# Kernel optimization log

Hardware: AMD Instinct MI355X
Metric: run time of the kernel (lower is better)

Reference implementation:

```python
import jax, jax.numpy as jnp
import numpy as np
from jax import lax

B, L, H, K = 64, 1024, 768, 4
C1, C2 = 0.1, 0.1


def crf_marginals(feats, maskf, T):
    """Batched linear-chain CRF forward-backward.
    feats: [B,L,K] emission scores, maskf: [B,L] float (1=valid), T: [K,K] transitions.
    Returns marginals [B,L,K] (zeroed at padded positions)."""
    a0 = feats[:, 0]  # [B,K]

    def fwd_step(a, xs):
        f_t, m_t = xs  # [B,K], [B]
        new = f_t + jax.nn.logsumexp(a[:, :, None] + T[None], axis=1)
        a = jnp.where(m_t[:, None] > 0, new, a)  # freeze alpha past last valid token
        return a, a

    _, alphas_rest = lax.scan(fwd_step, a0,
                              (jnp.swapaxes(feats[:, 1:], 0, 1), maskf[:, 1:].T))
    alphas = jnp.concatenate([a0[None], alphas_rest], axis=0)  # [L,B,K]
    logZ = jax.nn.logsumexp(alphas[-1], axis=-1)  # [B] (alpha frozen at last valid t)

    bL = jnp.zeros_like(a0)

    def bwd_step(b, xs):
        f_n, m_n = xs  # emission/mask at t+1
        new = jax.nn.logsumexp(T[None] + (f_n + b)[:, None, :], axis=2)
        b = jnp.where(m_n[:, None] > 0, new, b)  # beta stays 0 until last valid token
        return b, b

    xs = (jnp.swapaxes(feats[:, 1:][:, ::-1], 0, 1), maskf[:, 1:][:, ::-1].T)
    _, betas_rev = lax.scan(bwd_step, bL, xs)
    betas = jnp.concatenate([bL[None], betas_rev], axis=0)[::-1]  # [L,B,K]

    marg = jnp.exp(alphas + betas - logZ[None, :, None]) * maskf.T[:, :, None]
    return jnp.swapaxes(marg, 0, 1)  # [B,L,K]


def _forward(hidden, maskf, w, b, T):
    feats = hidden @ w.T + b                      # [B,L,K] feat2tri
    marg = crf_marginals(feats, maskf, T)
    sp = marg[:, :, 1]                            # select_polarities, masked [B,L]
    gamma = sp.sum(axis=1) / 2.0                  # [B]
    sent_vs = jnp.einsum('bl,blh->bh', sp, hidden) / gamma[:, None]
    s_prob = sp / gamma[:, None]                  # padded-ragged per-token probs
    s_prob_norm = jnp.abs(s_prob).sum(axis=1).mean()
    pena = jax.nn.relu(T[1, 0] - T[0, 0]) + jax.nn.relu(T[0, 1] - T[1, 1])
    norm_pen = C1 * pena + C2 * s_prob_norm
    return sent_vs, norm_pen, s_prob


def setup_inputs():
    key = jax.random.key(0)
    ks = jax.random.split(key, 8)
    hidden = jax.random.normal(ks[0], (B, L, H), dtype=jnp.float32)
    seq_lens = jax.random.randint(ks[1], (B,), L // 4, L + 1)
    # hidden_mask: 0 for valid tokens, nonzero for padding (forward uses mask = hidden_mask==0)
    hidden_mask = (jnp.arange(L)[None, :] >= seq_lens[:, None]).astype(jnp.int32)
    subj_position = jax.random.randint(ks[2], (B, L), -20, 21)
    obj_position = jax.random.randint(ks[3], (B, L), -20, 21)
    pe_inputs = jax.random.randint(ks[4], (B, L), 0, 2 * L)
    pe_binary = jax.random.randint(ks[5], (B, L), 0, 2)
    w_feat2tri = jax.random.normal(ks[6], (K, H), dtype=jnp.float32) * (1.0 / np.sqrt(H)).astype(np.float32)
    b_feat2tri = jnp.zeros((K,), dtype=jnp.float32)
    transitions = jax.random.normal(ks[7], (K, K), dtype=jnp.float32) * 0.1
    return dict(hidden=hidden, hidden_mask=hidden_mask, subj_position=subj_position,
                obj_position=obj_position, seq_lens=seq_lens, pe_inputs=pe_inputs,
                pe_binary=pe_binary, w_feat2tri=w_feat2tri, b_feat2tri=b_feat2tri,
                transitions=transitions)


def reference(hidden, hidden_mask, subj_position, obj_position, seq_lens, pe_inputs,
              pe_binary, w_feat2tri, b_feat2tri, transitions):
    maskf = (hidden_mask == 0).astype(hidden.dtype)
    # relevance is computed in the original forward but never consumed downstream,
    # so it has no effect on outputs; omitted here.
    return _forward(hidden, maskf, w_feat2tri, b_feat2tri, transitions)
```

## Files before the change

kernel.cpp:

```cpp
#include <hip/hip_runtime.h>

#define B 64
#define L 1024
#define H 768
#define NROWS (B * L)
#define LOG2E 1.4426950408889634f
#define CS 16
#define NCH 64
#define NG 16

#define EXP2(x) __builtin_amdgcn_exp2f(x)
#define LOG2(x) __builtin_amdgcn_logf(x)

__device__ __forceinline__ void renorm4(float& x0, float& x1, float& x2, float& x3, float& lc) {
    const float g = fmaxf(fmaxf(x0, x1), fmaxf(x2, x3));
    const int e = (__float_as_int(g) >> 23) & 255;
    const float s = __int_as_float((254 - e) << 23);
    x0 *= s; x1 *= s; x2 *= s; x3 *= s;
    lc += (float)(e - 127);
}

__global__ __launch_bounds__(256) void feats_kernel(
    const float* __restrict__ hidden, const float* __restrict__ w,
    const float* __restrict__ bias, float4* __restrict__ pfeatsT)
{
    const int lane = threadIdx.x & 63;
    const int wave = (blockIdx.x * blockDim.x + threadIdx.x) >> 6;
    const int nwaves = (gridDim.x * blockDim.x) >> 6;

    float wr[3][4][4];
#pragma unroll
    for (int c = 0; c < 3; ++c)
#pragma unroll
        for (int j = 0; j < 4; ++j)
#pragma unroll
            for (int k = 0; k < 4; ++k)
                wr[c][j][k] = w[k * H + lane * 4 + 256 * c + j];
    const float bb0 = bias[0], bb1 = bias[1], bb2 = bias[2], bb3 = bias[3];

    for (int row = wave; row < NROWS; row += nwaves) {
        const float4* hrow = reinterpret_cast<const float4*>(hidden) + (size_t)row * (H / 4);
        float acc[4] = {0.f, 0.f, 0.f, 0.f};
#pragma unroll
        for (int c = 0; c < 3; ++c) {
            float4 h = hrow[lane + 64 * c];
            const float hv[4] = {h.x, h.y, h.z, h.w};
#pragma unroll
            for (int j = 0; j < 4; ++j)
#pragma unroll
                for (int k = 0; k < 4; ++k)
                    acc[k] = fmaf(hv[j], wr[c][j][k], acc[k]);
        }
#pragma unroll
        for (int k = 0; k < 4; ++k) {
            float v = acc[k];
#pragma unroll
            for (int s = 32; s >= 1; s >>= 1) v += __shfl_xor(v, s, 64);
            acc[k] = v;
        }
        if (lane == 0) {
            const int b = row >> 10, l = row & 1023;
            pfeatsT[l * B + b] = make_float4(EXP2((acc[0] + bb0) * LOG2E),
                                             EXP2((acc[1] + bb1) * LOG2E),
                                             EXP2((acc[2] + bb2) * LOG2E),
                                             EXP2((acc[3] + bb3) * LOG2E));
        }
    }
}

__global__ __launch_bounds__(128) void chunkmat_kernel(
    const float4* __restrict__ pfeatsT, const int* __restrict__ seq_lens,
    const float* __restrict__ T, float* __restrict__ mats_p,
    float* __restrict__ mats_lc)
{
    const int b = threadIdx.x & 63;
    const int dir = threadIdx.x >> 6;
    const int c = blockIdx.x;
    const int sl = seq_lens[b];
    const int lo = c * CS + 1;
    const int hi = min(c * CS + CS, L - 1);
    const int ns = hi - lo + 1;

    float eT2[4][4];
#pragma unroll
    for (int i = 0; i < 4; ++i)
#pragma unroll
        for (int j = 0; j < 4; ++j) eT2[i][j] = EXP2(T[i * 4 + j] * LOG2E);

    float4 fr[CS];
#pragma unroll
    for (int u = 0; u < CS; ++u) {
        const int t = dir ? max(hi - u, lo) : min(lo + u, hi);
        fr[u] = pfeatsT[t * B + b];
    }

    float M[4][4];
#pragma unroll
    for (int i = 0; i < 4; ++i)
#pragma unroll
        for (int j = 0; j < 4; ++j) M[i][j] = (i == j) ? 1.f : 0.f;
    float lc = 0.f;

#pragma unroll
    for (int u = 0; u < CS; ++u) {
        const int pos = dir ? (hi - u) : (lo + u);
        const bool valid = (u < ns) && (pos < sl);
        const float f[4] = {fr[u].x, fr[u].y, fr[u].z, fr[u].w};
        float nM[4][4];
        if (dir == 0) {
#pragma unroll
            for (int i = 0; i < 4; ++i)
#pragma unroll
                for (int j = 0; j < 4; ++j) {
                    const float s = (M[i][0] * eT2[0][j] + M[i][1] * eT2[1][j]) +
                                    (M[i][2] * eT2[2][j] + M[i][3] * eT2[3][j]);
                    nM[i][j] = s * f[j];
                }
        } else {
            float Mg[4][4];
#pragma unroll
            for (int k = 0; k < 4; ++k)
#pragma unroll
                for (int j = 0; j < 4; ++j) Mg[k][j] = f[k] * M[k][j];
#pragma unroll
            for (int i = 0; i < 4; ++i)
#pragma unroll
                for (int j = 0; j < 4; ++j)
                    nM[i][j] = (eT2[i][0] * Mg[0][j] + eT2[i][1] * Mg[1][j]) +
                               (eT2[i][2] * Mg[2][j] + eT2[i][3] * Mg[3][j]);
        }
#pragma unroll
        for (int i = 0; i < 4; ++i)
#pragma unroll
            for (int j = 0; j < 4; ++j) M[i][j] = valid ? nM[i][j] : M[i][j];

        if (u == 7 || u == CS - 1) {
            float g = 0.f;
#pragma unroll
            for (int i = 0; i < 4; ++i)
#pragma unroll
                for (int j = 0; j < 4; ++j) g = fmaxf(g, M[i][j]);
            const int e = (__float_as_int(g) >> 23) & 255;
            const float s = __int_as_float((254 - e) << 23);
#pragma unroll
            for (int i = 0; i < 4; ++i)
#pragma unroll
                for (int j = 0; j < 4; ++j) M[i][j] *= s;
            lc += (float)(e - 127);
        }
    }
#pragma unroll
    for (int i = 0; i < 4; ++i)
#pragma unroll
        for (int j = 0; j < 4; ++j)
            mats_p[((dir * NCH + c) * 16 + i * 4 + j) * B + b] = M[i][j];
    mats_lc[(dir * NCH + c) * B + b] = lc;
}

__global__ __launch_bounds__(128) void groupmat_kernel(
    const float* __restrict__ mats_p, const float* __restrict__ mats_lc,
    float* __restrict__ smats_p, float* __restrict__ smats_lc)
{
    const int b = threadIdx.x & 63;
    const int dir = threadIdx.x >> 6;
    const int g = blockIdx.x;

    float P[4][4];
    float lc = 0.f;
    {
        const int c0 = 4 * g;
#pragma unroll
        for (int k = 0; k < 16; ++k)
            P[k >> 2][k & 3] = mats_p[((dir * NCH + c0) * 16 + k) * B + b];
        lc = mats_lc[(dir * NCH + c0) * B + b];
    }

#pragma unroll
    for (int q = 1; q < 4; ++q) {
        const int c = 4 * g + q;
        float Q[4][4];
#pragma unroll
        for (int k = 0; k < 16; ++k)
            Q[k >> 2][k & 3] = mats_p[((dir * NCH + c) * 16 + k) * B + b];
        lc += mats_lc[(dir * NCH + c) * B + b];

        float R[4][4];
#pragma unroll
        for (int i = 0; i < 4; ++i)
#pragma unroll
            for (int j = 0; j < 4; ++j)
                R[i][j] = (P[i][0] * Q[0][j] + P[i][1] * Q[1][j]) +
                          (P[i][2] * Q[2][j] + P[i][3] * Q[3][j]);

        float gmax = 0.f;
#pragma unroll
        for (int i = 0; i < 4; ++i)
#pragma unroll
            for (int j = 0; j < 4; ++j) gmax = fmaxf(gmax, R[i][j]);
        const int e = (__float_as_int(gmax) >> 23) & 255;
        const float s = __int_as_float((254 - e) << 23);
#pragma unroll
        for (int i = 0; i < 4; ++i)
#pragma unroll
            for (int j = 0; j < 4; ++j) P[i][j] = R[i][j] * s;
        lc += (float)(e - 127);
    }

#pragma unroll
    for (int i = 0; i < 4; ++i)
#pragma unroll
        for (int j = 0; j < 4; ++j)
            smats_p[((dir * NG + g) * 16 + i * 4 + j) * B + b] = P[i][j];
    smats_lc[(dir * NG + g) * B + b] = lc;
}

__global__ __launch_bounds__(128) void bound_kernel(
    const float4* __restrict__ pfeatsT, const float* __restrict__ smats_p,
    const float* __restrict__ smats_lc, float* __restrict__ gbound_p,
    float* __restrict__ gbound_lc, float* __restrict__ logZ)
{
    const int b = threadIdx.x & 63;
    const int dir = threadIdx.x >> 6;

    float Ms[4][17];
#pragma unroll
    for (int p = 0; p < 3; ++p) {
        const int cc = dir ? (NG - 1 - p) : p;
#pragma unroll
        for (int k = 0; k < 16; ++k)
            Ms[p][k] = smats_p[((dir * NG + cc) * 16 + k) * B + b];
        Ms[p][16] = smats_lc[(dir * NG + cc) * B + b];
    }

    float v0, v1, v2, v3, vlc = 0.f;
    if (dir == 0) {
        const float4 f0 = pfeatsT[b];
        v0 = f0.x; v1 = f0.y; v2 = f0.z; v3 = f0.w;
    } else {
        v0 = v1 = v2 = v3 = 1.f;
    }

#pragma unroll
    for (int u = 0; u < NG; ++u) {
        const int cc = dir ? (NG - 1 - u) : u;
        gbound_p[((dir * NG + cc) * 4 + 0) * B + b] = v0;
        gbound_p[((dir * NG + cc) * 4 + 1) * B + b] = v1;
        gbound_p[((dir * NG + cc) * 4 + 2) * B + b] = v2;
        gbound_p[((dir * NG + cc) * 4 + 3) * B + b] = v3;
        gbound_lc[(dir * NG + cc) * B + b] = vlc;
        if (u + 3 < NG) {
            const int cp = dir ? (NG - 1 - (u + 3)) : (u + 3);
#pragma unroll
            for (int k = 0; k < 16; ++k)
                Ms[(u + 3) & 3][k] = smats_p[((dir * NG + cp) * 16 + k) * B + b];
            Ms[(u + 3) & 3][16] = smats_lc[(dir * NG + cp) * B + b];
        }
        const float* Pm = Ms[u & 3];
        float n0, n1, n2, n3;
        if (dir == 0) {
            n0 = (v0 * Pm[0] + v1 * Pm[4]) + (v2 * Pm[8] + v3 * Pm[12]);
            n1 = (v0 * Pm[1] + v1 * Pm[5]) + (v2 * Pm[9] + v3 * Pm[13]);
            n2 = (v0 * Pm[2] + v1 * Pm[6]) + (v2 * Pm[10] + v3 * Pm[14]);
            n3 = (v0 * Pm[3] + v1 * Pm[7]) + (v2 * Pm[11] + v3 * Pm[15]);
        } else {
            n0 = (Pm[0] * v0 + Pm[1] * v1) + (Pm[2] * v2 + Pm[3] * v3);
            n1 = (Pm[4] * v0 + Pm[5] * v1) + (Pm[6] * v2 + Pm[7] * v3);
            n2 = (Pm[8] * v0 + Pm[9] * v1) + (Pm[10] * v2 + Pm[11] * v3);
            n3 = (Pm[12] * v0 + Pm[13] * v1) + (Pm[14] * v2 + Pm[15] * v3);
        }
        v0 = n0; v1 = n1; v2 = n2; v3 = n3;
        vlc += Pm[16];
        renorm4(v0, v1, v2, v3, vlc);
    }
    if (dir == 0)
        logZ[b] = LOG2(((v0 + v1) + (v2 + v3))) + vlc;
}

__global__ __launch_bounds__(128) void rescan_sp_kernel(
    const float4* __restrict__ pfeatsT, const int* __restrict__ seq_lens,
    const float* __restrict__ T, const float* __restrict__ mats_p,
    const float* __restrict__ mats_lc, const float* __restrict__ gbound_p,
    const float* __restrict__ gbound_lc, const float* __restrict__ logZ,
    float* __restrict__ spu, float* __restrict__ chunksum)
{
    const int tid = threadIdx.x;
    const int b = tid & 63;
    const int dir = tid >> 6;
    const int c = blockIdx.x;
    const int g = c >> 2;
    const int r = c & 3;
    const int sl = seq_lens[b];
    const int base = c * CS;

    float eT2[4][4];
#pragma unroll
    for (int i = 0; i < 4; ++i)
#pragma unroll
        for (int j = 0; j < 4; ++j) eT2[i][j] = EXP2(T[i * 4 + j] * LOG2E);

    __shared__ float ldb_p[CS * 64];
    __shared__ float ldb_lc[CS * 64];

    if (dir == 1) {
        float v0 = gbound_p[((NG + g) * 4 + 0) * B + b];
        float v1 = gbound_p[((NG + g) * 4 + 1) * B + b];
        float v2 = gbound_p[((NG + g) * 4 + 2) * B + b];
        float v3 = gbound_p[((NG + g) * 4 + 3) * B + b];
        float blc = gbound_lc[(NG + g) * B + b];
        for (int q = 3; q > r; --q) {
            const int cq = 4 * g + q;
            float Mq[16];
#pragma unroll
            for (int k = 0; k < 16; ++k)
                Mq[k] = mats_p[((NCH + cq) * 16 + k) * B + b];
            blc += mats_lc[(NCH + cq) * B + b];
            const float n0 = (Mq[0] * v0 + Mq[1] * v1) + (Mq[2] * v2 + Mq[3] * v3);
            const float n1 = (Mq[4] * v0 + Mq[5] * v1) + (Mq[6] * v2 + Mq[7] * v3);
            const float n2 = (Mq[8] * v0 + Mq[9] * v1) + (Mq[10] * v2 + Mq[11] * v3);
            const float n3 = (Mq[12] * v0 + Mq[13] * v1) + (Mq[14] * v2 + Mq[15] * v3);
            v0 = n0; v1 = n1; v2 = n2; v3 = n3;
            renorm4(v0, v1, v2, v3, blc);
        }

        const bool last = (c == NCH - 1);
        const int hi_n = last ? (L - 1) : (base + CS);
        const int cnt = last ? (CS - 1) : CS;
        if (last) { ldb_p[15 * 64 + b] = v1; ldb_lc[15 * 64 + b] = blc; }
        float4 fr[CS];
#pragma unroll
        for (int u = 0; u < CS; ++u) fr[u] = pfeatsT[max(hi_n - u, base + 1) * B + b];
#pragma unroll
        for (int u = 0; u < CS; ++u) {
            if (u < cnt) {
                const int n = hi_n - u;
                const bool valid = n < sl;
                const float4 f = fr[u];
                const float c0 = f.x * v0, c1 = f.y * v1, c2 = f.z * v2, c3 = f.w * v3;
                const float n0 = (eT2[0][0] * c0 + eT2[0][1] * c1) + (eT2[0][2] * c2 + eT2[0][3] * c3);
                const float n1 = (eT2[1][0] * c0 + eT2[1][1] * c1) + (eT2[1][2] * c2 + eT2[1][3] * c3);
                const float n2 = (eT2[2][0] * c0 + eT2[2][1] * c1) + (eT2[2][2] * c2 + eT2[2][3] * c3);
                const float n3 = (eT2[3][0] * c0 + eT2[3][1] * c1) + (eT2[3][2] * c2 + eT2[3][3] * c3);
                v0 = valid ? n0 : v0; v1 = valid ? n1 : v1;
                v2 = valid ? n2 : v2; v3 = valid ? n3 : v3;
                if ((u & 3) == 3) renorm4(v0, v1, v2, v3, blc);
                ldb_p[(n - 1 - base) * 64 + b] = v1;
                ldb_lc[(n - 1 - base) * 64 + b] = blc;
            }
        }
    }

    float av_p[CS], av_lc[CS];
    if (dir == 0) {
        float a0 = gbound_p[(g * 4 + 0) * B + b];
        float a1 = gbound_p[(g * 4 + 1) * B + b];
        float a2 = gbound_p[(g * 4 + 2) * B + b];
        float a3 = gbound_p[(g * 4 + 3) * B + b];
        float alc = gbound_lc[g * B + b];
        for (int q = 0; q < r; ++q) {
            const int cq = 4 * g + q;
            float Mq[16];
#pragma unroll
            for (int k = 0; k < 16; ++k)
                Mq[k] = mats_p[(cq * 16 + k) * B + b];
            alc += mats_lc[cq * B + b];
            const float n0 = (a0 * Mq[0] + a1 * Mq[4]) + (a2 * Mq[8] + a3 * Mq[12]);
            const float n1 = (a0 * Mq[1] + a1 * Mq[5]) + (a2 * Mq[9] + a3 * Mq[13]);
            const float n2 = (a0 * Mq[2] + a1 * Mq[6]) + (a2 * Mq[10] + a3 * Mq[14]);
            const float n3 = (a0 * Mq[3] + a1 * Mq[7]) + (a2 * Mq[11] + a3 * Mq[15]);
            a0 = n0; a1 = n1; a2 = n2; a3 = n3;
            renorm4(a0, a1, a2, a3, alc);
        }

        av_p[0] = a1; av_lc[0] = alc;
        float4 fr[CS - 1];
#pragma unroll
        for (int u = 1; u < CS; ++u) fr[u - 1] = pfeatsT[(base + u) * B + b];
#pragma unroll
        for (int u = 1; u < CS; ++u) {
            const int t = base + u;
            const bool valid = t < sl;
            const float4 f = fr[u - 1];
            const float s0 = (a0 * eT2[0][0] + a1 * eT2[1][0]) + (a2 * eT2[2][0] + a3 * eT2[3][0]);
            const float s1 = (a0 * eT2[0][1] + a1 * eT2[1][1]) + (a2 * eT2[2][1] + a3 * eT2[3][1]);
            const float s2 = (a0 * eT2[0][2] + a1 * eT2[1][2]) + (a2 * eT2[2][2] + a3 * eT2[3][2]);
            const float s3 = (a0 * eT2[0][3] + a1 * eT2[1][3]) + (a2 * eT2[2][3] + a3 * eT2[3][3]);
            const float n0 = s0 * f.x, n1 = s1 * f.y, n2 = s2 * f.z, n3 = s3 * f.w;
            a0 = valid ? n0 : a0; a1 = valid ? n1 : a1;
            a2 = valid ? n2 : a2; a3 = valid ? n3 : a3;
            if ((u & 3) == 3) renorm4(a0, a1, a2, a3, alc);
            av_p[u] = a1; av_lc[u] = alc;
        }
    }

    __syncthreads();

    if (dir == 0) {
        const float lz = logZ[b];
        float sp[CS];
        float local = 0.f;
#pragma unroll
        for (int u = 0; u < CS; ++u) {
            const int l = base + u;
            const float x = (l < sl)
                ? av_p[u] * ldb_p[u * 64 + b] * EXP2(av_lc[u] + ldb_lc[u * 64 + b] - lz)
                : 0.f;
            sp[u] = x;
            local += x;
        }
        float4* dst = reinterpret_cast<float4*>(spu + b * L + base);
#pragma unroll
        for (int q = 0; q < 4; ++q)
            dst[q] = make_float4(sp[4 * q], sp[4 * q + 1], sp[4 * q + 2], sp[4 * q + 3]);
        chunksum[c * 64 + b] = local;
    }
}

__global__ __launch_bounds__(1024) void sentv_final_kernel(
    const float* __restrict__ hidden, const float* __restrict__ spu,
    const float* __restrict__ chunksum, const float* __restrict__ T,
    float* __restrict__ out, float* __restrict__ sprob)
{
    const int hc = blockIdx.x;
    const int b  = blockIdx.y;
    const int tid = threadIdx.x;
    const int lane = tid & 63;
    const int w = tid >> 6;

    __shared__ float s_tot;
    if (tid < 64) {
        float v = chunksum[tid * 64 + b];
#pragma unroll
        for (int s = 32; s >= 1; s >>= 1) v += __shfl_xor(v, s, 64);
        if (tid == 0) s_tot = v;
    }
    __syncthreads();
    const float inv = 2.0f / s_tot;

    const float4* hb = reinterpret_cast<const float4*>(hidden) +
                       (size_t)b * L * (H / 4) + hc * 64;
    const float* sp = spu + b * L;

    float4 acc = make_float4(0.f, 0.f, 0.f, 0.f);
#pragma unroll 8
    for (int i = 0; i < 64; ++i) {
        const int l = w + 16 * i;
        const float s = sp[l];
        const float4 h = hb[(size_t)l * (H / 4) + lane];
        acc.x = fmaf(s, h.x, acc.x); acc.y = fmaf(s, h.y, acc.y);
        acc.z = fmaf(s, h.z, acc.z); acc.w = fmaf(s, h.w, acc.w);
    }

    __shared__ float4 red[16][64];
    red[w][lane] = acc;
    __syncthreads();
    if (tid < 64) {
        float4 r = make_float4(0.f, 0.f, 0.f, 0.f);
#pragma unroll
        for (int q = 0; q < 16; q += 4) {
            const float4 a0 = red[q][lane], a1 = red[q + 1][lane];
            const float4 a2 = red[q + 2][lane], a3 = red[q + 3][lane];
            r.x += (a0.x + a1.x) + (a2.x + a3.x);
            r.y += (a0.y + a1.y) + (a2.y + a3.y);
            r.z += (a0.z + a1.z) + (a2.z + a3.z);
            r.w += (a0.w + a1.w) + (a2.w + a3.w);
        }
        r.x *= inv; r.y *= inv; r.z *= inv; r.w *= inv;
        reinterpret_cast<float4*>(out)[(size_t)b * (H / 4) + hc * 64 + lane] = r;
    }

    if (hc == 0) {
        sprob[b * L + tid] = sp[tid] * inv;
        if (b == 0 && tid == 0) {
            const float pena = fmaxf(T[4] - T[0], 0.f) + fmaxf(T[1] - T[5], 0.f);
            out[B * H] = 0.1f * pena + 0.1f * 2.0f;
        }
    }
}

extern "C" void kernel_launch(void* const* d_in, const int* in_sizes, int n_in,
                              void* d_out, int out_size, void* d_ws, size_t ws_size,
                              hipStream_t stream) {
    const float* hidden   = (const float*)d_in[0];
    const int*   seq_lens = (const int*)d_in[4];
    const float* w        = (const float*)d_in[7];
    const float* bias     = (const float*)d_in[8];
    const float* T        = (const float*)d_in[9];

    float* ws = (float*)d_ws;
    float4* pfeatsT    = (float4*)(ws);
    float*  mats_p     = ws + 262144;
    float*  mats_lc    = ws + 393216;
    float*  smats_p    = ws + 401408;
    float*  smats_lc   = ws + 434176;
    float*  gbound_p   = ws + 436224;
    float*  gbound_lc  = ws + 444416;
    float*  logZ       = ws + 446464;
    float*  chunksum   = ws + 446528;
    float*  spu        = ws + 450624;

    float* out   = (float*)d_out;
    float* sprob = out + B * H + 1;

    feats_kernel<<<2048, 256, 0, stream>>>(hidden, w, bias, pfeatsT);
    chunkmat_kernel<<<NCH, 128, 0, stream>>>((const float4*)pfeatsT, seq_lens, T, mats_p, mats_lc);
    groupmat_kernel<<<NG, 128, 0, stream>>>(mats_p, mats_lc, smats_p, smats_lc);
    bound_kernel<<<1, 128, 0, stream>>>((const float4*)pfeatsT, smats_p, smats_lc,
                                        gbound_p, gbound_lc, logZ);
    rescan_sp_kernel<<<NCH, 128, 0, stream>>>((const float4*)pfeatsT, seq_lens, T,
                                              mats_p, mats_lc, gbound_p, gbound_lc,
                                              logZ, spu, chunksum);
    sentv_final_kernel<<<dim3(3, 64), 1024, 0, stream>>>(hidden, spu, chunksum, T, out, sprob);
}
```

Measured before the change: 85.94 us.

## Fuse chunk, group and boundary CRF kernels via last-block atomic counters

Merges the chunk-matrix, group-matrix and boundary-scan kernels into one launch. The last block to finish each group of four chunks, found with an atomic counter, composes the group matrix, and the last group block runs the boundary scan. Counters are zeroed in the feats kernel. This removes two kernel launches and their inter-kernel gaps, at the cost of atomics, threadfences and serialized tail work inside one kernel.

```diff
diff --git a/kernel.cpp b/kernel.cpp
--- a/kernel.cpp
+++ b/kernel.cpp
@@ -22,8 +22,11 @@
 
 __global__ __launch_bounds__(256) void feats_kernel(
     const float* __restrict__ hidden, const float* __restrict__ w,
-    const float* __restrict__ bias, float4* __restrict__ pfeatsT)
+    const float* __restrict__ bias, float4* __restrict__ pfeatsT,
+    unsigned* __restrict__ counters)
 {
+    if (blockIdx.x == 0 && threadIdx.x < 17) counters[threadIdx.x] = 0u;
+
     const int lane = threadIdx.x & 63;
     const int wave = (blockIdx.x * blockDim.x + threadIdx.x) >> 6;
     const int nwaves = (gridDim.x * blockDim.x) >> 6;
@@ -68,18 +71,20 @@
     }
 }
 
-__global__ __launch_bounds__(128) void chunkmat_kernel(
+__global__ __launch_bounds__(128) void crfmid_kernel(
     const float4* __restrict__ pfeatsT, const int* __restrict__ seq_lens,
     const float* __restrict__ T, float* __restrict__ mats_p,
-    float* __restrict__ mats_lc)
+    float* __restrict__ mats_lc, float* __restrict__ smats_p,
+    float* __restrict__ smats_lc, float* __restrict__ gbound_p,
+    float* __restrict__ gbound_lc, float* __restrict__ logZ,
+    unsigned* __restrict__ counters)
 {
-    const int b = threadIdx.x & 63;
-    const int dir = threadIdx.x >> 6;
+    const int tid = threadIdx.x;
+    const int b = tid & 63;
+    const int dir = tid >> 6;
     const int c = blockIdx.x;
+    const int g = c >> 2;
     const int sl = seq_lens[b];
-    const int lo = c * CS + 1;
-    const int hi = min(c * CS + CS, L - 1);
-    const int ns = hi - lo + 1;
 
     float eT2[4][4];
 #pragma unroll
@@ -87,193 +92,206 @@
 #pragma unroll
         for (int j = 0; j < 4; ++j) eT2[i][j] = EXP2(T[i * 4 + j] * LOG2E);
 
-    float4 fr[CS];
-#pragma unroll
-    for (int u = 0; u < CS; ++u) {
-        const int t = dir ? max(hi - u, lo) : min(lo + u, hi);
-        fr[u] = pfeatsT[t * B + b];
-    }
-
-    float M[4][4];
-#pragma unroll
-    for (int i = 0; i < 4; ++i)
-#pragma unroll
-        for (int j = 0; j < 4; ++j) M[i][j] = (i == j) ? 1.f : 0.f;
-    float lc = 0.f;
-
-#pragma unroll
-    for (int u = 0; u < CS; ++u) {
-        const int pos = dir ? (hi - u) : (lo + u);
-        const bool valid = (u < ns) && (pos < sl);
-        const float f[4] = {fr[u].x, fr[u].y, fr[u].z, fr[u].w};
-        float nM[4][4];
+    {
+        const int lo = c * CS + 1;
+        const int hi = min(c * CS + CS, L - 1);
+        const int ns = hi - lo + 1;
+
+        float4 fr[CS];
+#pragma unroll
+        for (int u = 0; u < CS; ++u) {
+            const int t = dir ? max(hi - u, lo) : min(lo + u, hi);
+            fr[u] = pfeatsT[t * B + b];
+        }
+
+        float M[4][4];
+#pragma unroll
+        for (int i = 0; i < 4; ++i)
+#pragma unroll
+            for (int j = 0; j < 4; ++j) M[i][j] = (i == j) ? 1.f : 0.f;
+        float lc = 0.f;
+
+#pragma unroll
+        for (int u = 0; u < CS; ++u) {
+            const int pos = dir ? (hi - u) : (lo + u);
+            const bool valid = (u < ns) && (pos < sl);
+            const float f[4] = {fr[u].x, fr[u].y, fr[u].z, fr[u].w};
+            float nM[4][4];
+            if (dir == 0) {
+#pragma unroll
+                for (int i = 0; i < 4; ++i)
+#pragma unroll
+                    for (int j = 0; j < 4; ++j) {
+                        const float s = (M[i][0] * eT2[0][j] + M[i][1] * eT2[1][j]) +
+                                        (M[i][2] * eT2[2][j] + M[i][3] * eT2[3][j]);
+                        nM[i][j] = s * f[j];
+                    }
+            } else {
+                float Mg[4][4];
+#pragma unroll
+                for (int k = 0; k < 4; ++k)
+#pragma unroll
+                    for (int j = 0; j < 4; ++j) Mg[k][j] = f[k] * M[k][j];
+#pragma unroll
+                for (int i = 0; i < 4; ++i)
+#pragma unroll
+                    for (int j = 0; j < 4; ++j)
+                        nM[i][j] = (eT2[i][0] * Mg[0][j] + eT2[i][1] * Mg[1][j]) +
+                                   (eT2[i][2] * Mg[2][j] + eT2[i][3] * Mg[3][j]);
+            }
+#pragma unroll
+            for (int i = 0; i < 4; ++i)
+#pragma unroll
+                for (int j = 0; j < 4; ++j) M[i][j] = valid ? nM[i][j] : M[i][j];
+
+            if (u == 7 || u == CS - 1) {
+                float gm = 0.f;
+#pragma unroll
+                for (int i = 0; i < 4; ++i)
+#pragma unroll
+                    for (int j = 0; j < 4; ++j) gm = fmaxf(gm, M[i][j]);
+                const int e = (__float_as_int(gm) >> 23) & 255;
+                const float s = __int_as_float((254 - e) << 23);
+#pragma unroll
+                for (int i = 0; i < 4; ++i)
+#pragma unroll
+                    for (int j = 0; j < 4; ++j) M[i][j] *= s;
+                lc += (float)(e - 127);
+            }
+        }
+#pragma unroll
+        for (int i = 0; i < 4; ++i)
+#pragma unroll
+            for (int j = 0; j < 4; ++j)
+                mats_p[((dir * NCH + c) * 16 + i * 4 + j) * B + b] = M[i][j];
+        mats_lc[(dir * NCH + c) * B + b] = lc;
+    }
+
+    __syncthreads();
+    __threadfence();
+    __shared__ int amLast;
+    if (tid == 0) {
+        const unsigned old = __hip_atomic_fetch_add(&counters[g], 1u,
+                                                    __ATOMIC_ACQ_REL, __HIP_MEMORY_SCOPE_AGENT);
+        amLast = (old == 3u);
+    }
+    __syncthreads();
+    if (!amLast) return;
+    __threadfence();
+
+    {
+        float P[4][4];
+        float lc;
+        {
+            const int c0 = 4 * g;
+#pragma unroll
+            for (int k = 0; k < 16; ++k)
+                P[k >> 2][k & 3] = mats_p[((dir * NCH + c0) * 16 + k) * B + b];
+            lc = mats_lc[(dir * NCH + c0) * B + b];
+        }
+#pragma unroll
+        for (int q = 1; q < 4; ++q) {
+            const int cc = 4 * g + q;
+            float Q[4][4];
+#pragma unroll
+            for (int k = 0; k < 16; ++k)
+                Q[k >> 2][k & 3] = mats_p[((dir * NCH + cc) * 16 + k) * B + b];
+            lc += mats_lc[(dir * NCH + cc) * B + b];
+
+            float R[4][4];
+#pragma unroll
+            for (int i = 0; i < 4; ++i)
+#pragma unroll
+                for (int j = 0; j < 4; ++j)
+                    R[i][j] = (P[i][0] * Q[0][j] + P[i][1] * Q[1][j]) +
+                              (P[i][2] * Q[2][j] + P[i][3] * Q[3][j]);
+
+            float gmax = 0.f;
+#pragma unroll
+            for (int i = 0; i < 4; ++i)
+#pragma unroll
+                for (int j = 0; j < 4; ++j) gmax = fmaxf(gmax, R[i][j]);
+            const int e = (__float_as_int(gmax) >> 23) & 255;
+            const float s = __int_as_float((254 - e) << 23);
+#pragma unroll
+            for (int i = 0; i < 4; ++i)
+#pragma unroll
+                for (int j = 0; j < 4; ++j) P[i][j] = R[i][j] * s;
+            lc += (float)(e - 127);
+        }
+#pragma unroll
+        for (int i = 0; i < 4; ++i)
+#pragma unroll
+            for (int j = 0; j < 4; ++j)
+                smats_p[((dir * NG + g) * 16 + i * 4 + j) * B + b] = P[i][j];
+        smats_lc[(dir * NG + g) * B + b] = lc;
+    }
+
+    __syncthreads();
+    __threadfence();
+    if (tid == 0) {
+        const unsigned old = __hip_atomic_fetch_add(&counters[16], 1u,
+                                                    __ATOMIC_ACQ_REL, __HIP_MEMORY_SCOPE_AGENT);
+        amLast = (old == 15u);
+    }
+    __syncthreads();
+    if (!amLast) return;
+    __threadfence();
+
+    {
+        float Ms[4][17];
+#pragma unroll
+        for (int p = 0; p < 3; ++p) {
+            const int cc = dir ? (NG - 1 - p) : p;
+#pragma unroll
+            for (int k = 0; k < 16; ++k)
+                Ms[p][k] = smats_p[((dir * NG + cc) * 16 + k) * B + b];
+            Ms[p][16] = smats_lc[(dir * NG + cc) * B + b];
+        }
+
+        float v0, v1, v2, v3, vlc = 0.f;
         if (dir == 0) {
-#pragma unroll
-            for (int i = 0; i < 4; ++i)
-#pragma unroll
-                for (int j = 0; j < 4; ++j) {
-                    const float s = (M[i][0] * eT2[0][j] + M[i][1] * eT2[1][j]) +
-                                    (M[i][2] * eT2[2][j] + M[i][3] * eT2[3][j]);
-                    nM[i][j] = s * f[j];
-                }
+            const float4 f0 = pfeatsT[b];
+            v0 = f0.x; v1 = f0.y; v2 = f0.z; v3 = f0.w;
         } else {
-            float Mg[4][4];
-#pragma unroll
-            for (int k = 0; k < 4; ++k)
-#pragma unroll
-                for (int j = 0; j < 4; ++j) Mg[k][j] = f[k] * M[k][j];
-#pragma unroll
-            for (int i = 0; i < 4; ++i)
-#pragma unroll
-                for (int j = 0; j < 4; ++j)
-                    nM[i][j] = (eT2[i][0] * Mg[0][j] + eT2[i][1] * Mg[1][j]) +
-                               (eT2[i][2] * Mg[2][j] + eT2[i][3] * Mg[3][j]);
-        }
-#pragma unroll
-        for (int i = 0; i < 4; ++i)
-#pragma unroll
-            for (int j = 0; j < 4; ++j) M[i][j] = valid ? nM[i][j] : M[i][j];
-
-        if (u == 7 || u == CS - 1) {
-            float g = 0.f;
-#pragma unroll
-            for (int i = 0; i < 4; ++i)
-#pragma unroll
-                for (int j = 0; j < 4; ++j) g = fmaxf(g, M[i][j]);
-            const int e = (__float_as_int(g) >> 23) & 255;
-            const float s = __int_as_float((254 - e) << 23);
-#pragma unroll
-            for (int i = 0; i < 4; ++i)
-#pragma unroll
-                for (int j = 0; j < 4; ++j) M[i][j] *= s;
-            lc += (float)(e - 127);
-        }
-    }
-#pragma unroll
-    for (int i = 0; i < 4; ++i)
-#pragma unroll
-        for (int j = 0; j < 4; ++j)
-            mats_p[((dir * NCH + c) * 16 + i * 4 + j) * B + b] = M[i][j];
-    mats_lc[(dir * NCH + c) * B + b] = lc;
-}
-
-__global__ __launch_bounds__(128) void groupmat_kernel(
-    const float* __restrict__ mats_p, const float* __restrict__ mats_lc,
-    float* __restrict__ smats_p, float* __restrict__ smats_lc)
-{
-    const int b = threadIdx.x & 63;
-    const int dir = threadIdx.x >> 6;
-    const int g = blockIdx.x;
-
-    float P[4][4];
-    float lc = 0.f;
-    {
-        const int c0 = 4 * g;
-#pragma unroll
-        for (int k = 0; k < 16; ++k)
-            P[k >> 2][k & 3] = mats_p[((dir * NCH + c0) * 16 + k) * B + b];
-        lc = mats_lc[(dir * NCH + c0) * B + b];
-    }
-
-#pragma unroll
-    for (int q = 1; q < 4; ++q) {
-        const int c = 4 * g + q;
-        float Q[4][4];
-#pragma unroll
-        for (int k = 0; k < 16; ++k)
-            Q[k >> 2][k & 3] = mats_p[((dir * NCH + c) * 16 + k) * B + b];
-        lc += mats_lc[(dir * NCH + c) * B + b];
-
-        float R[4][4];
-#pragma unroll
-        for (int i = 0; i < 4; ++i)
-#pragma unroll
-            for (int j = 0; j < 4; ++j)
-                R[i][j] = (P[i][0] * Q[0][j] + P[i][1] * Q[1][j]) +
-                          (P[i][2] * Q[2][j] + P[i][3] * Q[3][j]);
-
-        float gmax = 0.f;
-#pragma unroll
-        for (int i = 0; i < 4; ++i)
-#pragma unroll
-            for (int j = 0; j < 4; ++j) gmax = fmaxf(gmax, R[i][j]);
-        const int e = (__float_as_int(gmax) >> 23) & 255;
-        const float s = __int_as_float((254 - e) << 23);
-#pragma unroll
-        for (int i = 0; i < 4; ++i)
-#pragma unroll
-            for (int j = 0; j < 4; ++j) P[i][j] = R[i][j] * s;
-        lc += (float)(e - 127);
-    }
-
-#pragma unroll
-    for (int i = 0; i < 4; ++i)
-#pragma unroll
-        for (int j = 0; j < 4; ++j)
-            smats_p[((dir * NG + g) * 16 + i * 4 + j) * B + b] = P[i][j];
-    smats_lc[(dir * NG + g) * B + b] = lc;
-}
-
-__global__ __launch_bounds__(128) void bound_kernel(
-    const float4* __restrict__ pfeatsT, const float* __restrict__ smats_p,
-    const float* __restrict__ smats_lc, float* __restrict__ gbound_p,
-    float* __restrict__ gbound_lc, float* __restrict__ logZ)
-{
-    const int b = threadIdx.x & 63;
-    const int dir = threadIdx.x >> 6;
-
-    float Ms[4][17];
-#pragma unroll
-    for (int p = 0; p < 3; ++p) {
-        const int cc = dir ? (NG - 1 - p) : p;
-#pragma unroll
-        for (int k = 0; k < 16; ++k)
-            Ms[p][k] = smats_p[((dir * NG + cc) * 16 + k) * B + b];
-        Ms[p][16] = smats_lc[(dir * NG + cc) * B + b];
-    }
-
-    float v0, v1, v2, v3, vlc = 0.f;
-    if (dir == 0) {
-        const float4 f0 = pfeatsT[b];
-        v0 = f0.x; v1 = f0.y; v2 = f0.z; v3 = f0.w;
-    } else {
-        v0 = v1 = v2 = v3 = 1.f;
-    }
-
-#pragma unroll
-    for (int u = 0; u < NG; ++u) {
-        const int cc = dir ? (NG - 1 - u) : u;
-        gbound_p[((dir * NG + cc) * 4 + 0) * B + b] = v0;
-        gbound_p[((dir * NG + cc) * 4 + 1) * B + b] = v1;
-        gbound_p[((dir * NG + cc) * 4 + 2) * B + b] = v2;
-        gbound_p[((dir * NG + cc) * 4 + 3) * B + b] = v3;
-        gbound_lc[(dir * NG + cc) * B + b] = vlc;
-        if (u + 3 < NG) {
-            const int cp = dir ? (NG - 1 - (u + 3)) : (u + 3);
-#pragma unroll
-            for (int k = 0; k < 16; ++k)
-                Ms[(u + 3) & 3][k] = smats_p[((dir * NG + cp) * 16 + k) * B + b];
-            Ms[(u + 3) & 3][16] = smats_lc[(dir * NG + cp) * B + b];
-        }
-        const float* Pm = Ms[u & 3];
-        float n0, n1, n2, n3;
-        if (dir == 0) {
-            n0 = (v0 * Pm[0] + v1 * Pm[4]) + (v2 * Pm[8] + v3 * Pm[12]);
-            n1 = (v0 * Pm[1] + v1 * Pm[5]) + (v2 * Pm[9] + v3 * Pm[13]);
-            n2 = (v0 * Pm[2] + v1 * Pm[6]) + (v2 * Pm[10] + v3 * Pm[14]);
-            n3 = (v0 * Pm[3] + v1 * Pm[7]) + (v2 * Pm[11] + v3 * Pm[15]);
-        } else {
-            n0 = (Pm[0] * v0 + Pm[1] * v1) + (Pm[2] * v2 + Pm[3] * v3);
-            n1 = (Pm[4] * v0 + Pm[5] * v1) + (Pm[6] * v2 + Pm[7] * v3);
-            n2 = (Pm[8] * v0 + Pm[9] * v1) + (Pm[10] * v2 + Pm[11] * v3);
-            n3 = (Pm[12] * v0 + Pm[13] * v1) + (Pm[14] * v2 + Pm[15] * v3);
-        }
-        v0 = n0; v1 = n1; v2 = n2; v3 = n3;
-        vlc += Pm[16];
-        renorm4(v0, v1, v2, v3, vlc);
-    }
-    if (dir == 0)
-        logZ[b] = LOG2(((v0 + v1) + (v2 + v3))) + vlc;
+            v0 = v1 = v2 = v3 = 1.f;
+        }
+
+#pragma unroll
+        for (int u = 0; u < NG; ++u) {
+            const int cc = dir ? (NG - 1 - u) : u;
+            gbound_p[((dir * NG + cc) * 4 + 0) * B + b] = v0;
+            gbound_p[((dir * NG + cc) * 4 + 1) * B + b] = v1;
+            gbound_p[((dir * NG + cc) * 4 + 2) * B + b] = v2;
+            gbound_p[((dir * NG + cc) * 4 + 3) * B + b] = v3;
+            gbound_lc[(dir * NG + cc) * B + b] = vlc;
+            if (u + 3 < NG) {
+                const int cp = dir ? (NG - 1 - (u + 3)) : (u + 3);
+#pragma unroll
+                for (int k = 0; k < 16; ++k)
+                    Ms[(u + 3) & 3][k] = smats_p[((dir * NG + cp) * 16 + k) * B + b];
+                Ms[(u + 3) & 3][16] = smats_lc[(dir * NG + cp) * B + b];
+            }
+            const float* Pm = Ms[u & 3];
+            float n0, n1, n2, n3;
+            if (dir == 0) {
+                n0 = (v0 * Pm[0] + v1 * Pm[4]) + (v2 * Pm[8] + v3 * Pm[12]);
+                n1 = (v0 * Pm[1] + v1 * Pm[5]) + (v2 * Pm[9] + v3 * Pm[13]);
+                n2 = (v0 * Pm[2] + v1 * Pm[6]) + (v2 * Pm[10] + v3 * Pm[14]);
+                n3 = (v0 * Pm[3] + v1 * Pm[7]) + (v2 * Pm[11] + v3 * Pm[15]);
+            } else {
+                n0 = (Pm[0] * v0 + Pm[1] * v1) + (Pm[2] * v2 + Pm[3] * v3);
+                n1 = (Pm[4] * v0 + Pm[5] * v1) + (Pm[6] * v2 + Pm[7] * v3);
+                n2 = (Pm[8] * v0 + Pm[9] * v1) + (Pm[10] * v2 + Pm[11] * v3);
+                n3 = (Pm[12] * v0 + Pm[13] * v1) + (Pm[14] * v2 + Pm[15] * v3);
+            }
+            v0 = n0; v1 = n1; v2 = n2; v3 = n3;
+            vlc += Pm[16];
+            renorm4(v0, v1, v2, v3, vlc);
+        }
+        if (dir == 0)
+            logZ[b] = LOG2(((v0 + v1) + (v2 + v3))) + vlc;
+    }
 }
 
 __global__ __launch_bounds__(128) void rescan_sp_kernel(
@@ -487,25 +505,25 @@
     const float* T        = (const float*)d_in[9];
 
     float* ws = (float*)d_ws;
-    float4* pfeatsT    = (float4*)(ws);
-    float*  mats_p     = ws + 262144;
-    float*  mats_lc    = ws + 393216;
-    float*  smats_p    = ws + 401408;
-    float*  smats_lc   = ws + 434176;
-    float*  gbound_p   = ws + 436224;
-    float*  gbound_lc  = ws + 444416;
-    float*  logZ       = ws + 446464;
-    float*  chunksum   = ws + 446528;
-    float*  spu        = ws + 450624;
+    float4*   pfeatsT    = (float4*)(ws);
+    float*    mats_p     = ws + 262144;
+    float*    mats_lc    = ws + 393216;
+    float*    smats_p    = ws + 401408;
+    float*    smats_lc   = ws + 434176;
+    float*    gbound_p   = ws + 436224;
+    float*    gbound_lc  = ws + 444416;
+    float*    logZ       = ws + 446464;
+    float*    chunksum   = ws + 446528;
+    float*    spu        = ws + 450624;
+    unsigned* counters   = (unsigned*)(ws + 516160);
 
     float* out   = (float*)d_out;
     float* sprob = out + B * H + 1;
 
-    feats_kernel<<<2048, 256, 0, stream>>>(hidden, w, bias, pfeatsT);
-    chunkmat_kernel<<<NCH, 128, 0, stream>>>((const float4*)pfeatsT, seq_lens, T, mats_p, mats_lc);
-    groupmat_kernel<<<NG, 128, 0, stream>>>(mats_p, mats_lc, smats_p, smats_lc);
-    bound_kernel<<<1, 128, 0, stream>>>((const float4*)pfeatsT, smats_p, smats_lc,
-                                        gbound_p, gbound_lc, logZ);
+    feats_kernel<<<2048, 256, 0, stream>>>(hidden, w, bias, pfeatsT, counters);
+    crfmid_kernel<<<NCH, 128, 0, stream>>>((const float4*)pfeatsT, seq_lens, T,
+                                           mats_p, mats_lc, smats_p, smats_lc,
+                                           gbound_p, gbound_lc, logZ, counters);
     rescan_sp_kernel<<<NCH, 128, 0, stream>>>((const float4*)pfeatsT, seq_lens, T,
                                               mats_p, mats_lc, gbound_p, gbound_lc,
                                               logZ, spu, chunksum);
```

After: 92.55 us. +7.7%, slower.
